# Kernel tuning notes

Hardware: AMD Instinct MI355X
Metric: run time of the kernel (lower is better)

The kernel has to match this reference:

```python
import jax, jax.numpy as jnp
import numpy as np

B, C, F, H = 262144, 16, 16, 12   # batch, n_clusters, cluster_size, ceil(0.75*F)
HH = 12                           # head hidden = ceil(0.75*C)
EPS = 1e-16


def _linear_init(key, shape, fan_in):
    # torch nn.Linear default: U(-1/sqrt(fan_in), 1/sqrt(fan_in))
    bound = 1.0 / np.sqrt(fan_in)
    return jax.random.uniform(key, shape, jnp.float32, -bound, bound)


def setup_inputs() -> dict:
    key = jax.random.key(0)
    ks = jax.random.split(key, 9)
    x = jax.random.normal(ks[0], (B, C * F), dtype=jnp.float32)
    cluster_idx = jnp.arange(C * F, dtype=jnp.int32).reshape(C, F)
    # Tail autoencoders, stacked over clusters (torch Linear layout [out,in])
    We = _linear_init(ks[1], (C, H, F), F)   # encoder weight per cluster
    be = _linear_init(ks[2], (C, H), F)      # encoder bias
    Wd = _linear_init(ks[3], (C, F, H), H)   # decoder weight per cluster
    bd = _linear_init(ks[4], (C, F), H)      # decoder bias
    # Head autoencoder
    He = _linear_init(ks[5], (HH, C), C)
    hbe = _linear_init(ks[6], (HH,), C)
    Hd = _linear_init(ks[7], (C, HH), HH)
    hbd = _linear_init(ks[8], (C,), HH)
    return {"x": x, "We": We, "be": be, "Wd": Wd, "bd": bd,
            "He": He, "hbe": hbe, "Hd": Hd, "hbd": hbd,
            "cluster_idx": cluster_idx}


def reference(x, We, be, Wd, bd, He, hbe, Hd, hbd, cluster_idx):
    # Gather per-cluster features: [B, C, F]
    xc = x[:, cluster_idx]
    # Normalization with default norm params (min=0, max=1)
    xc = (xc - 0.0) / (1.0 - 0.0 + EPS)
    # Grouped tail autoencoders: sigmoid(Linear) twice, batched over clusters
    h = jax.nn.sigmoid(jnp.einsum('bcf,chf->bch', xc, We) + be)
    rec = jax.nn.sigmoid(jnp.einsum('bch,cfh->bcf', h, Wd) + bd)
    # Per-cluster RMSE over batch and features -> [C]
    loss = jnp.sqrt(jnp.mean((rec - xc) ** 2, axis=(0, 2)))
    loss = jnp.where(loss == 0.0, jnp.float32(0.01), loss)
    # Output normalization (min=0, max=1)
    tails = (loss - 0.0) / (1.0 - 0.0 + EPS)
    # Head autoencoder on the 1-D tail-loss vector
    h2 = jax.nn.sigmoid(He @ tails + hbe)
    head_out = jax.nn.sigmoid(Hd @ h2 + hbd)
    return head_out, tails
```

## Files before the change

kernel.cpp:

```cpp
#include <hip/hip_runtime.h>
#include <math.h>

#define NB      262144
#define NC      16
#define NF      16
#define NH      12
#define NHH     12
#define THREADS 256
#define BLOCKS  (NB / THREADS)

__device__ __forceinline__ float sigmoid_fast(float z) {
    float e = __expf(-z);
    return __builtin_amdgcn_rcpf(1.0f + e);
}

__global__ __launch_bounds__(THREADS) void ae_main(
    const float* __restrict__ x,
    const float* __restrict__ We,
    const float* __restrict__ be,
    const float* __restrict__ Wd,
    const float* __restrict__ bd,
    float* __restrict__ partials)
{
    const int tid  = threadIdx.x;
    const int lane = tid & 63;
    const int wave = tid >> 6;
    const size_t b = (size_t)blockIdx.x * THREADS + tid;

    __shared__ float wred[NC][4];

    const float* xrow = x + b * (NC * NF);

    #pragma unroll 1
    for (int c = 0; c < NC; ++c) {
        float xc[NF];
        const float4* xp = reinterpret_cast<const float4*>(xrow + c * NF);
        #pragma unroll
        for (int k = 0; k < 4; ++k) {
            float4 v = xp[k];
            xc[4*k+0] = v.x; xc[4*k+1] = v.y; xc[4*k+2] = v.z; xc[4*k+3] = v.w;
        }

        const float* wec = We + c * (NH * NF);
        const float* bec = be + c * NH;
        float h[NH];
        #pragma unroll
        for (int hh = 0; hh < NH; ++hh) {
            float z = bec[hh];
            #pragma unroll
            for (int f = 0; f < NF; ++f)
                z = fmaf(xc[f], wec[hh * NF + f], z);
            h[hh] = sigmoid_fast(z);
        }

        const float* wdc = Wd + c * (NF * NH);
        const float* bdc = bd + c * NF;
        float lsum = 0.0f;
        #pragma unroll
        for (int f = 0; f < NF; ++f) {
            float z = bdc[f];
            #pragma unroll
            for (int hh = 0; hh < NH; ++hh)
                z = fmaf(h[hh], wdc[f * NH + hh], z);
            float r = sigmoid_fast(z);
            float d = r - xc[f];
            lsum = fmaf(d, d, lsum);
        }

        float v = lsum;
        #pragma unroll
        for (int off = 32; off > 0; off >>= 1)
            v += __shfl_down(v, off, 64);
        if (lane == 0) wred[c][wave] = v;
    }

    __syncthreads();
    if (tid < NC) {
        float s = wred[tid][0] + wred[tid][1] + wred[tid][2] + wred[tid][3];
        partials[(size_t)blockIdx.x * NC + tid] = s;
    }
}

__global__ __launch_bounds__(THREADS) void ae_final(
    const float* __restrict__ partials,
    const float* __restrict__ He,
    const float* __restrict__ hbe,
    const float* __restrict__ Hd,
    const float* __restrict__ hbd,
    float* __restrict__ out)
{
    __shared__ float red[NC][17];
    __shared__ float tails_s[NC];
    __shared__ float h2_s[NHH];

    const int tid = threadIdx.x;
    const int c = tid & 15;
    const int g = tid >> 4;

    float s = 0.0f;
    for (int i = g; i < BLOCKS; i += 16)
        s += partials[(size_t)i * NC + c];
    red[c][g] = s;
    __syncthreads();

    if (tid < NC) {
        float t = 0.0f;
        #pragma unroll
        for (int g2 = 0; g2 < 16; ++g2) t += red[tid][g2];
        float loss = sqrtf(t * (1.0f / 4194304.0f));
        if (loss == 0.0f) loss = 0.01f;
        tails_s[tid] = loss;
        out[16 + tid] = loss;
    }
    __syncthreads();

    if (tid < NHH) {
        float z = hbe[tid];
        #pragma unroll
        for (int cc = 0; cc < NC; ++cc)
            z = fmaf(He[tid * NC + cc], tails_s[cc], z);
        h2_s[tid] = 1.0f / (1.0f + __expf(-z));
    }
    __syncthreads();

    if (tid < NC) {
        float z = hbd[tid];
        #pragma unroll
        for (int j = 0; j < NHH; ++j)
            z = fmaf(Hd[tid * NHH + j], h2_s[j], z);
        out[tid] = 1.0f / (1.0f + __expf(-z));
    }
}

extern "C" void kernel_launch(void* const* d_in, const int* in_sizes, int n_in,
                              void* d_out, int out_size, void* d_ws, size_t ws_size,
                              hipStream_t stream) {
    const float* x   = (const float*)d_in[0];
    const float* We  = (const float*)d_in[1];
    const float* be  = (const float*)d_in[2];
    const float* Wd  = (const float*)d_in[3];
    const float* bd  = (const float*)d_in[4];
    const float* He  = (const float*)d_in[5];
    const float* hbe = (const float*)d_in[6];
    const float* Hd  = (const float*)d_in[7];
    const float* hbd = (const float*)d_in[8];

    float* out      = (float*)d_out;
    float* partials = (float*)d_ws;

    ae_main<<<BLOCKS, THREADS, 0, stream>>>(x, We, be, Wd, bd, partials);
    ae_final<<<1, THREADS, 0, stream>>>(partials, He, hbe, Hd, hbd, out);
}
```

Baseline: 454.5 us.

## Split clusters across a second grid dimension and prefetch next cluster's inputs

The main kernel now launches a 2-D grid in which each block handles 4 of the 16 clusters for its 256 rows, giving four times as many blocks. Inside the block the cluster loop is fully unrolled, with the next cluster's 64 bytes of x loaded into registers before the current cluster is computed. Launch bounds now request 8 blocks per SM. The partials layout and the final reduction indexing are changed to match. The aim is more parallelism and better latency hiding on the memory-bound x stream, at the cost of strided per-thread access to x across blocks and possible register pressure under the occupancy hint.

```diff
diff --git a/kernel.cpp b/kernel.cpp
--- a/kernel.cpp
+++ b/kernel.cpp
@@ -7,14 +7,16 @@
 #define NH      12
 #define NHH     12
 #define THREADS 256
-#define BLOCKS  (NB / THREADS)
+#define BX      (NB / THREADS)
+#define GY      4
+#define CPB     (NC / GY)
 
 __device__ __forceinline__ float sigmoid_fast(float z) {
     float e = __expf(-z);
     return __builtin_amdgcn_rcpf(1.0f + e);
 }
 
-__global__ __launch_bounds__(THREADS) void ae_main(
+__global__ __launch_bounds__(THREADS, 8) void ae_main(
     const float* __restrict__ x,
     const float* __restrict__ We,
     const float* __restrict__ be,
@@ -25,22 +27,27 @@
     const int tid  = threadIdx.x;
     const int lane = tid & 63;
     const int wave = tid >> 6;
+    const int c0   = blockIdx.y * CPB;
     const size_t b = (size_t)blockIdx.x * THREADS + tid;
 
-    __shared__ float wred[NC][4];
+    const float4* xp = reinterpret_cast<const float4*>(x + b * (NC * NF) + (size_t)c0 * NF);
 
-    const float* xrow = x + b * (NC * NF);
+    float acc[CPB];
+    float4 buf0 = xp[0], buf1 = xp[1], buf2 = xp[2], buf3 = xp[3];
 
-    #pragma unroll 1
-    for (int c = 0; c < NC; ++c) {
+    #pragma unroll
+    for (int j = 0; j < CPB; ++j) {
         float xc[NF];
-        const float4* xp = reinterpret_cast<const float4*>(xrow + c * NF);
-        #pragma unroll
-        for (int k = 0; k < 4; ++k) {
-            float4 v = xp[k];
-            xc[4*k+0] = v.x; xc[4*k+1] = v.y; xc[4*k+2] = v.z; xc[4*k+3] = v.w;
+        xc[0]=buf0.x; xc[1]=buf0.y; xc[2]=buf0.z; xc[3]=buf0.w;
+        xc[4]=buf1.x; xc[5]=buf1.y; xc[6]=buf1.z; xc[7]=buf1.w;
+        xc[8]=buf2.x; xc[9]=buf2.y; xc[10]=buf2.z; xc[11]=buf2.w;
+        xc[12]=buf3.x; xc[13]=buf3.y; xc[14]=buf3.z; xc[15]=buf3.w;
+        if (j + 1 < CPB) {
+            buf0 = xp[4*(j+1)+0]; buf1 = xp[4*(j+1)+1];
+            buf2 = xp[4*(j+1)+2]; buf3 = xp[4*(j+1)+3];
         }
 
+        const int c = c0 + j;
         const float* wec = We + c * (NH * NF);
         const float* bec = be + c * NH;
         float h[NH];
@@ -66,18 +73,22 @@
             float d = r - xc[f];
             lsum = fmaf(d, d, lsum);
         }
+        acc[j] = lsum;
+    }
 
-        float v = lsum;
+    __shared__ float wred[CPB][4];
+    #pragma unroll
+    for (int j = 0; j < CPB; ++j) {
+        float v = acc[j];
         #pragma unroll
         for (int off = 32; off > 0; off >>= 1)
             v += __shfl_down(v, off, 64);
-        if (lane == 0) wred[c][wave] = v;
+        if (lane == 0) wred[j][wave] = v;
     }
-
     __syncthreads();
-    if (tid < NC) {
+    if (tid < CPB) {
         float s = wred[tid][0] + wred[tid][1] + wred[tid][2] + wred[tid][3];
-        partials[(size_t)blockIdx.x * NC + tid] = s;
+        partials[((size_t)blockIdx.y * BX + blockIdx.x) * CPB + tid] = s;
     }
 }
 
@@ -96,10 +107,11 @@
     const int tid = threadIdx.x;
     const int c = tid & 15;
     const int g = tid >> 4;
+    const int by = c >> 2, jj = c & 3;
 
     float s = 0.0f;
-    for (int i = g; i < BLOCKS; i += 16)
-        s += partials[(size_t)i * NC + c];
+    for (int bx = g; bx < BX; bx += 16)
+        s += partials[((size_t)by * BX + bx) * CPB + jj];
     red[c][g] = s;
     __syncthreads();
 
@@ -148,6 +160,7 @@
     float* out      = (float*)d_out;
     float* partials = (float*)d_ws;
 
-    ae_main<<<BLOCKS, THREADS, 0, stream>>>(x, We, be, Wd, bd, partials);
+    dim3 grid(BX, GY);
+    ae_main<<<grid, THREADS, 0, stream>>>(x, We, be, Wd, bd, partials);
     ae_final<<<1, THREADS, 0, stream>>>(partials, He, hbe, Hd, hbd, out);
 }
```

Measured after the change: 486.4 us. 1.07x slower.

## Prefetch next cluster's inputs in registers and widen final reduction block

Applied to the files above, without the earlier changes.

The main kernel now loads the next cluster's 16 input floats into registers while computing the current cluster, a software pipeline meant to hide global load latency behind the encoder/decoder arithmetic. The final reduction kernel is launched with 1024 threads and 64 groups per cluster instead of 16, to shorten its serial loop over the partials. The prefetch raises register pressure, and the last iteration issues a redundant load.

```diff
diff --git a/kernel.cpp b/kernel.cpp
--- a/kernel.cpp
+++ b/kernel.cpp
@@ -7,7 +7,7 @@
 #define NH      12
 #define NHH     12
 #define THREADS 256
-#define BLOCKS  (NB / THREADS)
+#define BX      (NB / THREADS)
 
 __device__ __forceinline__ float sigmoid_fast(float z) {
     float e = __expf(-z);
@@ -29,17 +29,20 @@
 
     __shared__ float wred[NC][4];
 
-    const float* xrow = x + b * (NC * NF);
+    const float4* xp = reinterpret_cast<const float4*>(x + b * (NC * NF));
+
+    float4 b0 = xp[0], b1 = xp[1], b2 = xp[2], b3 = xp[3];
 
     #pragma unroll 1
     for (int c = 0; c < NC; ++c) {
         float xc[NF];
-        const float4* xp = reinterpret_cast<const float4*>(xrow + c * NF);
-        #pragma unroll
-        for (int k = 0; k < 4; ++k) {
-            float4 v = xp[k];
-            xc[4*k+0] = v.x; xc[4*k+1] = v.y; xc[4*k+2] = v.z; xc[4*k+3] = v.w;
-        }
+        xc[0]=b0.x;  xc[1]=b0.y;  xc[2]=b0.z;  xc[3]=b0.w;
+        xc[4]=b1.x;  xc[5]=b1.y;  xc[6]=b1.z;  xc[7]=b1.w;
+        xc[8]=b2.x;  xc[9]=b2.y;  xc[10]=b2.z; xc[11]=b2.w;
+        xc[12]=b3.x; xc[13]=b3.y; xc[14]=b3.z; xc[15]=b3.w;
+
+        const int cn = (c + 1 < NC) ? (c + 1) : c;
+        b0 = xp[4*cn+0]; b1 = xp[4*cn+1]; b2 = xp[4*cn+2]; b3 = xp[4*cn+3];
 
         const float* wec = We + c * (NH * NF);
         const float* bec = be + c * NH;
@@ -67,11 +70,10 @@
             lsum = fmaf(d, d, lsum);
         }
 
-        float v = lsum;
         #pragma unroll
         for (int off = 32; off > 0; off >>= 1)
-            v += __shfl_down(v, off, 64);
-        if (lane == 0) wred[c][wave] = v;
+            lsum += __shfl_down(lsum, off, 64);
+        if (lane == 0) wred[c][wave] = lsum;
     }
 
     __syncthreads();
@@ -81,7 +83,7 @@
     }
 }
 
-__global__ __launch_bounds__(THREADS) void ae_final(
+__global__ __launch_bounds__(1024) void ae_final(
     const float* __restrict__ partials,
     const float* __restrict__ He,
     const float* __restrict__ hbe,
@@ -89,7 +91,7 @@
     const float* __restrict__ hbd,
     float* __restrict__ out)
 {
-    __shared__ float red[NC][17];
+    __shared__ float red[NC][65];
     __shared__ float tails_s[NC];
     __shared__ float h2_s[NHH];
 
@@ -98,15 +100,15 @@
     const int g = tid >> 4;
 
     float s = 0.0f;
-    for (int i = g; i < BLOCKS; i += 16)
-        s += partials[(size_t)i * NC + c];
+    for (int bx = g; bx < BX; bx += 64)
+        s += partials[(size_t)bx * NC + c];
     red[c][g] = s;
     __syncthreads();
 
     if (tid < NC) {
         float t = 0.0f;
         #pragma unroll
-        for (int g2 = 0; g2 < 16; ++g2) t += red[tid][g2];
+        for (int g2 = 0; g2 < 64; ++g2) t += red[tid][g2];
         float loss = sqrtf(t * (1.0f / 4194304.0f));
         if (loss == 0.0f) loss = 0.01f;
         tails_s[tid] = loss;
@@ -148,6 +150,6 @@
     float* out      = (float*)d_out;
     float* partials = (float*)d_ws;
 
-    ae_main<<<BLOCKS, THREADS, 0, stream>>>(x, We, be, Wd, bd, partials);
-    ae_final<<<1, THREADS, 0, stream>>>(partials, He, hbe, Hd, hbd, out);
+    ae_main<<<BX, THREADS, 0, stream>>>(x, We, be, Wd, bd, partials);
+    ae_final<<<1, 1024, 0, stream>>>(partials, He, hbe, Hd, hbd, out);
 }
```

Result: no change. 452.7 us (-0.4%).
